# Optimization experiments

Hardware: AMD Instinct MI355X
Metric: run time of the kernel (lower is better)

Reference implementation:

```python
import jax, jax.numpy as jnp
import numpy as np

FFT_LEN = 512
FFT_BINS = FFT_LEN // 2 + 1  # 257


def _dft_kernels(fft_len):
    n = np.arange(fft_len)
    k = np.arange(fft_len // 2 + 1).reshape(-1, 1)
    ang = 2.0 * np.pi * k * n / fft_len
    real_kernel = jnp.asarray(np.cos(ang), dtype=jnp.float32)   # (bins, fft_len)
    imag_kernel = jnp.asarray(-np.sin(ang), dtype=jnp.float32)  # (bins, fft_len)
    return real_kernel, imag_kernel


def setup_inputs() -> dict:
    key = jax.random.key(0)
    x = jax.random.normal(key, (16, 4000, FFT_LEN), dtype=jnp.float32)
    real_kernel, imag_kernel = _dft_kernels(FFT_LEN)
    return {"x": x, "real_kernel": real_kernel, "imag_kernel": imag_kernel}


def reference(x, real_kernel, imag_kernel):
    # x: (B, F, N); kernels: (K, N) with K = N//2 + 1
    B, F, _ = x.shape
    real = jnp.einsum("bfn,kn->bfk", x, real_kernel)  # (B, F, K)
    imag = jnp.einsum("bfn,kn->bfk", x, imag_kernel)  # (B, F, K)
    # interleave real/imag per frequency bin: [..., r0, i0, r1, i1, ...]
    out = jnp.stack([real, imag], axis=-1).reshape(B, F, -1)  # (B, F, 2K)
    return out
```

## Files before the change

### kernel.cpp

```cpp
#include <hip/hip_runtime.h>

typedef _Float16 f16x8 __attribute__((ext_vector_type(8)));
typedef float f32x4 __attribute__((ext_vector_type(4)));

#define MDIM 64000
#define KDIM 512
#define NCOLS 514
#define NPAD 512
#define BM 128
#define BN 128
#define BK 32
#define KT (KDIM / BK)
#define NT 4
#define NWG 2000

#define GLOAD_LDS16(g, l)                                        \
  __builtin_amdgcn_global_load_lds(                              \
      (const __attribute__((address_space(1))) void*)(g),        \
      (__attribute__((address_space(3))) void*)(l), 16, 0, 0)

__global__ void prep_w(const float* __restrict__ rk, const float* __restrict__ ik,
                       _Float16* __restrict__ wb) {
  int n = blockIdx.x;
  int k = threadIdx.x;
  int bin = n >> 1;
  const float* src = (n & 1) ? ik : rk;
  wb[(size_t)n * KDIM + k] = (_Float16)src[bin * KDIM + k];
}

__global__ __launch_bounds__(256, 3)
void dft_gemm(const float* __restrict__ x, const _Float16* __restrict__ wb,
              float* __restrict__ out) {
  __shared__ float As[2][BM * BK];
  __shared__ _Float16 Bs[2][BN * BK];

  const int tid = threadIdx.x;
  const int l   = tid & 63;
  const int w   = tid >> 6;
  const int lr  = l & 15;
  const int lg  = l >> 4;
  const int wm  = (w >> 1) * 64;
  const int wn  = (w & 1) * 64;

  const int wgid = (blockIdx.x & 7) * (NWG / 8) + (blockIdx.x >> 3);
  const int mt = wgid >> 2;
  const int nt = wgid & 3;
  const int m0 = mt * BM;
  const int n0 = nt * BN;

  f32x4 acc[4][4] = {};
  float nyq = 0.0f;

  const int arow0 = w * 32 + (l >> 3);
  const float* asrc = x + (size_t)(m0 + arow0) * KDIM + (((l & 7) ^ (l >> 3)) << 2);

  const int brow0 = w * 32 + (l >> 2);
  const _Float16* bsrc =
      wb + (size_t)(n0 + brow0) * KDIM + (((l & 3) ^ ((l >> 3) & 3)) << 3);

#define STAGE(t, b)                                                     \
  {                                                                     \
    _Pragma("unroll")                                                   \
    for (int s = 0; s < 4; ++s)                                         \
      GLOAD_LDS16(asrc + (size_t)s * 8 * KDIM + (t) * BK,              \
                  &As[b][(w * 32 + s * 8) * BK]);                       \
    _Pragma("unroll")                                                   \
    for (int s = 0; s < 2; ++s)                                         \
      GLOAD_LDS16(bsrc + (size_t)s * 16 * KDIM + (t) * BK,             \
                  &Bs[b][(w * 32 + s * 16) * BK]);                      \
  }

#define COMPUTE(b)                                                     \
  {                                                                    \
    f16x8 av[4], bv[4];                                                \
    _Pragma("unroll")                                                  \
    for (int fm = 0; fm < 4; ++fm) {                                   \
      int row = wm + fm * 16 + lr;                                     \
      int sw  = lr & 7;                                     \
      int c0  = lg * 2;                                                \
      f32x4 lo = *reinterpret_cast<const f32x4*>(                      \
          &As[b][row * BK + ((c0 ^ sw) << 2)]);                        \
      f32x4 hi = *reinterpret_cast<const f32x4*>(                      \
          &As[b][row * BK + (((c0 + 1) ^ sw) << 2)]);                  \
      f16x8 h;                                                         \
      h[0] = (_Float16)lo[0]; h[1] = (_Float16)lo[1];                  \
      h[2] = (_Float16)lo[2]; h[3] = (_Float16)lo[3];                  \
      h[4] = (_Float16)hi[0]; h[5] = (_Float16)hi[1];                  \
      h[6] = (_Float16)hi[2]; h[7] = (_Float16)hi[3];                  \
      av[fm] = h;                                                      \
    }                                                                  \
    _Pragma("unroll")                                                  \
    for (int fn = 0; fn < 4; ++fn) {                                   \
      int row = wn + fn * 16 + lr;                                     \
      int c   = lg ^ ((lr >> 1) & 3);                  \
      bv[fn] = *reinterpret_cast<const f16x8*>(&Bs[b][row * BK + (c << 3)]); \
    }                                                                  \
    _Pragma("unroll")                                                  \
    for (int fm = 0; fm < 4; ++fm)                                     \
      _Pragma("unroll")                                                \
      for (int fn = 0; fn < 4; ++fn)                                   \
        acc[fm][fn] = __builtin_amdgcn_mfma_f32_16x16x32_f16(          \
            av[fm], bv[fn], acc[fm][fn], 0, 0, 0);                     \
  }

  const int nrow = tid >> 1;
#define NYQ(b)                                                         \
  {                                                                    \
    _Pragma("unroll")                                                  \
    for (int j = 0; j < 4; ++j) {                                      \
      int c = ((tid & 1) * 4 + j) ^ (nrow & 7);                        \
      f32x4 v = *reinterpret_cast<const f32x4*>(&As[b][nrow * BK + (c << 2)]); \
      nyq += (v[0] - v[1]) + (v[2] - v[3]);                            \
    }                                                                  \
  }

  STAGE(0, 0);
  __syncthreads();

  int b = 0;
  for (int t = 0; t < KT; ++t) {
    if (t + 1 < KT) STAGE(t + 1, b ^ 1);
    COMPUTE(b);
    if (nt == 0) NYQ(b);
    __syncthreads();
    b ^= 1;
  }

#pragma unroll
  for (int fm = 0; fm < 4; ++fm) {
#pragma unroll
    for (int rr = 0; rr < 4; ++rr) {
      int row = m0 + wm + fm * 16 + lg * 4 + rr;
      size_t base = (size_t)row * NCOLS;
#pragma unroll
      for (int fn = 0; fn < 4; ++fn)
        out[base + n0 + wn + fn * 16 + lr] = acc[fm][fn][rr];
    }
  }

  if (nt == 0) {
    float tot = nyq + __shfl_xor(nyq, 1);
    if ((tid & 1) == 0) {
      size_t base = (size_t)(m0 + nrow) * NCOLS;
      out[base + 512] = tot;
      out[base + 513] = 0.0f;
    }
  }
#undef STAGE
#undef COMPUTE
#undef NYQ
}

extern "C" void kernel_launch(void* const* d_in, const int* in_sizes, int n_in,
                              void* d_out, int out_size, void* d_ws, size_t ws_size,
                              hipStream_t stream) {
  const float* x  = (const float*)d_in[0];
  const float* rk = (const float*)d_in[1];
  const float* ik = (const float*)d_in[2];
  float* out = (float*)d_out;
  _Float16* wb = (_Float16*)d_ws;

  prep_w<<<dim3(NPAD), dim3(KDIM), 0, stream>>>(rk, ik, wb);

  dim3 grid(NWG);
  dft_gemm<<<grid, dim3(256), 0, stream>>>(x, wb, out);
}
```

Measured before the change: 90.84 us.

## Triple-buffer A tiles with prefetch distance two and explicit vmcnt waits

Splits staging of A and B tiles, gives the fp32 A tile three LDS buffers so it is prefetched two iterations ahead, and swaps __syncthreads for partial s_waitcnt vmcnt plus s_barrier so loads stay in flight across iterations. The aim is to hide global-load latency on the streaming x input. The larger LDS footprint lowers the launch-bounds occupancy hint from 3 to 2 blocks per CU, which risks weaker latency hiding through concurrent workgroups.

```diff
diff --git a/kernel.cpp b/kernel.cpp
--- a/kernel.cpp
+++ b/kernel.cpp
@@ -28,25 +28,22 @@
   wb[(size_t)n * KDIM + k] = (_Float16)src[bin * KDIM + k];
 }
 
-__global__ __launch_bounds__(256, 3)
+__global__ __launch_bounds__(256, 2)
 void dft_gemm(const float* __restrict__ x, const _Float16* __restrict__ wb,
               float* __restrict__ out) {
-  __shared__ float As[2][BM * BK];
+  __shared__ float As[3][BM * BK];
   __shared__ _Float16 Bs[2][BN * BK];
 
   const int tid = threadIdx.x;
   const int l   = tid & 63;
   const int w   = tid >> 6;
-  const int lr  = l & 15;
-  const int lg  = l >> 4;
+  const int lr  = l & 15, lg = l >> 4;
   const int wm  = (w >> 1) * 64;
   const int wn  = (w & 1) * 64;
 
   const int wgid = (blockIdx.x & 7) * (NWG / 8) + (blockIdx.x >> 3);
-  const int mt = wgid >> 2;
-  const int nt = wgid & 3;
-  const int m0 = mt * BM;
-  const int n0 = nt * BN;
+  const int mt = wgid >> 2, nt = wgid & 3;
+  const int m0 = mt * BM, n0 = nt * BN;
 
   f32x4 acc[4][4] = {};
   float nyq = 0.0f;
@@ -58,19 +55,23 @@
   const _Float16* bsrc =
       wb + (size_t)(n0 + brow0) * KDIM + (((l & 3) ^ ((l >> 3) & 3)) << 3);
 
-#define STAGE(t, b)                                                     \
+#define STAGE_A(t, b)                                                   \
   {                                                                     \
     _Pragma("unroll")                                                   \
     for (int s = 0; s < 4; ++s)                                         \
       GLOAD_LDS16(asrc + (size_t)s * 8 * KDIM + (t) * BK,              \
                   &As[b][(w * 32 + s * 8) * BK]);                       \
+  }
+
+#define STAGE_B(t, b)                                                   \
+  {                                                                     \
     _Pragma("unroll")                                                   \
     for (int s = 0; s < 2; ++s)                                         \
       GLOAD_LDS16(bsrc + (size_t)s * 16 * KDIM + (t) * BK,             \
                   &Bs[b][(w * 32 + s * 16) * BK]);                      \
   }
 
-#define COMPUTE(b)                                                     \
+#define COMPUTE(ba, bbuf)                                              \
   {                                                                    \
     f16x8 av[4], bv[4];                                                \
     _Pragma("unroll")                                                  \
@@ -79,9 +80,9 @@
       int sw  = lr & 7;                                     \
       int c0  = lg * 2;                                                \
       f32x4 lo = *reinterpret_cast<const f32x4*>(                      \
-          &As[b][row * BK + ((c0 ^ sw) << 2)]);                        \
+          &As[ba][row * BK + ((c0 ^ sw) << 2)]);                       \
       f32x4 hi = *reinterpret_cast<const f32x4*>(                      \
-          &As[b][row * BK + (((c0 + 1) ^ sw) << 2)]);                  \
+          &As[ba][row * BK + (((c0 + 1) ^ sw) << 2)]);                 \
       f16x8 h;                                                         \
       h[0] = (_Float16)lo[0]; h[1] = (_Float16)lo[1];                  \
       h[2] = (_Float16)lo[2]; h[3] = (_Float16)lo[3];                  \
@@ -93,7 +94,7 @@
     for (int fn = 0; fn < 4; ++fn) {                                   \
       int row = wn + fn * 16 + lr;                                     \
       int c   = lg ^ ((lr >> 1) & 3);                  \
-      bv[fn] = *reinterpret_cast<const f16x8*>(&Bs[b][row * BK + (c << 3)]); \
+      bv[fn] = *reinterpret_cast<const f16x8*>(&Bs[bbuf][row * BK + (c << 3)]); \
     }                                                                  \
     _Pragma("unroll")                                                  \
     for (int fm = 0; fm < 4; ++fm)                                     \
@@ -104,26 +105,45 @@
   }
 
   const int nrow = tid >> 1;
-#define NYQ(b)                                                         \
+#define NYQ(ba)                                                        \
   {                                                                    \
     _Pragma("unroll")                                                  \
     for (int j = 0; j < 4; ++j) {                                      \
       int c = ((tid & 1) * 4 + j) ^ (nrow & 7);                        \
-      f32x4 v = *reinterpret_cast<const f32x4*>(&As[b][nrow * BK + (c << 2)]); \
+      f32x4 v = *reinterpret_cast<const f32x4*>(&As[ba][nrow * BK + (c << 2)]); \
       nyq += (v[0] - v[1]) + (v[2] - v[3]);                            \
     }                                                                  \
   }
 
-  STAGE(0, 0);
-  __syncthreads();
+  STAGE_B(0, 0);
+  __builtin_amdgcn_sched_barrier(0);
+  STAGE_A(0, 0);
+  __builtin_amdgcn_sched_barrier(0);
+  STAGE_A(1, 1);
+  __builtin_amdgcn_sched_barrier(0);
+  asm volatile("s_waitcnt vmcnt(4)");
+  __builtin_amdgcn_s_barrier();
+  __builtin_amdgcn_sched_barrier(0);
 
-  int b = 0;
   for (int t = 0; t < KT; ++t) {
-    if (t + 1 < KT) STAGE(t + 1, b ^ 1);
-    COMPUTE(b);
-    if (nt == 0) NYQ(b);
-    __syncthreads();
-    b ^= 1;
+    const int ba = t % 3, bbuf = t & 1;
+    if (t + 1 < KT) {
+      STAGE_B(t + 1, (t + 1) & 1);
+      __builtin_amdgcn_sched_barrier(0);
+    }
+    if (t + 2 < KT) {
+      STAGE_A(t + 2, (t + 2) % 3);
+      __builtin_amdgcn_sched_barrier(0);
+    }
+    COMPUTE(ba, bbuf);
+    if (nt == 0) NYQ(ba);
+    if (t + 1 < KT) {
+      __builtin_amdgcn_sched_barrier(0);
+      if (t < KT - 2) asm volatile("s_waitcnt vmcnt(4) lgkmcnt(0)");
+      else            asm volatile("s_waitcnt vmcnt(0) lgkmcnt(0)");
+      __builtin_amdgcn_s_barrier();
+      __builtin_amdgcn_sched_barrier(0);
+    }
   }
 
 #pragma unroll
@@ -146,7 +166,8 @@
       out[base + 513] = 0.0f;
     }
   }
-#undef STAGE
+#undef STAGE_A
+#undef STAGE_B
 #undef COMPUTE
 #undef NYQ
 }
```

Measured after the change: 93.95 us. 3.4% more time.
